# Performance work log

Hardware: AMD Instinct MI355X
Metric: run time of the kernel (lower is better)

## Reference

```python
import jax, jax.numpy as jnp
import numpy as np
import math

EPS = 1e-5
L2_EPS = 1e-12  # torch F.normalize default eps


def _bitlinear(x, W):
    """BitNet b1.58-style BitLinear: ternary weights (per-tensor mean-abs scale)
    and per-token int8 absmax activation quantization. No bias.
    x: [..., in], W: [out, in] -> [..., out]
    """
    w_scale = jnp.clip(jnp.mean(jnp.abs(W)), EPS, None)
    W_q = jnp.clip(jnp.round(W / w_scale), -1.0, 1.0) * w_scale
    x_scale = 127.0 / jnp.clip(jnp.max(jnp.abs(x), axis=-1, keepdims=True), EPS, None)
    x_q = jnp.clip(jnp.round(x * x_scale), -128.0, 127.0) / x_scale
    return jnp.einsum('bsi,oi->bso', x_q, W_q)


def setup_inputs() -> dict:
    key = jax.random.key(0)
    k1, k2, k3 = jax.random.split(key, 3)
    B, S, D_in, P, D_out = 4, 4096, 2048, 16, 2048
    x = jax.random.normal(k1, (B, S, D_in), dtype=jnp.float32)
    # xavier_normal_: std = sqrt(2 / (fan_in + fan_out))
    Wk = jax.random.normal(k2, (P, D_in), dtype=jnp.float32) * math.sqrt(2.0 / (D_in + P))
    Wv = jax.random.normal(k3, (D_out, P), dtype=jnp.float32) * math.sqrt(2.0 / (P + D_out))
    return {"x": x, "Wk": Wk, "Wv": Wv}


def reference(x, Wk, Wv):
    # key projection -> [B, S, P]
    attn = _bitlinear(x, Wk)
    # gelu (exact erf form, torch default) + L2-normalize * sqrt(P)
    attn = jax.nn.gelu(attn, approximate=False)
    norm = jnp.clip(jnp.linalg.norm(attn, axis=-1, keepdims=True), L2_EPS, None)
    attn = attn / norm * jnp.sqrt(jnp.float32(attn.shape[-1]))
    # value projection -> [B, S, D_out]
    return _bitlinear(attn, Wv)
```

## Files before the change

kernel.cpp:

```cpp
#include <hip/hip_runtime.h>

#define DIN   2048
#define DOUT  2048
#define NP    16
#define TPW   8
#define WPB   2

#define HDR_OFF   0
#define WK4_OFF   256
#define WV4_OFF   (WK4_OFF + 32768)

static __device__ __forceinline__ int dot4(unsigned a, unsigned b, int c) {
#if defined(__has_builtin) && __has_builtin(__builtin_amdgcn_sdot4)
  return __builtin_amdgcn_sdot4((int)a, (int)b, c, false);
#else
  c += (int)(signed char)(a & 0xffu)        * (int)(signed char)(b & 0xffu);
  c += (int)(signed char)((a >> 8) & 0xffu) * (int)(signed char)((b >> 8) & 0xffu);
  c += (int)(signed char)((a >> 16) & 0xffu)* (int)(signed char)((b >> 16) & 0xffu);
  c += (int)(signed char)(a >> 24)          * (int)(signed char)(b >> 24);
  return c;
#endif
}

static __device__ __forceinline__ unsigned qmagic(float f, float xs) {
  return __float_as_uint(fmaf(f, xs, 12582912.0f)) & 0xffu;
}

static __device__ __forceinline__ unsigned q8(float f, float xs) {
  float t = f * xs;
  float r = rintf(t);
  r = fmaxf(-128.0f, fminf(127.0f, r));
  return ((unsigned)(int)r) & 0xffu;
}

__global__ __launch_bounds__(256) void k_prep(
    const float* __restrict__ Wk, const float* __restrict__ Wv,
    float* __restrict__ hdr, unsigned* __restrict__ wk4, unsigned* __restrict__ wv4)
{
  __shared__ float red[8][256];
  const int tid = threadIdx.x, b = blockIdx.x;
  const int isV = (b >= 32);
  const float4* W = (const float4*)(isV ? Wv : Wk);

  float4 own = make_float4(0.f, 0.f, 0.f, 0.f);
#pragma unroll
  for (int lb = 0; lb < 8; ++lb) {
    float s = 0.f;
#pragma unroll
    for (int i = 0; i < 4; ++i) {
      float4 v = W[lb * 1024 + i * 256 + tid];
      if (!isV && (lb * 4 + i) == b) own = v;
      s += fabsf(v.x) + fabsf(v.y) + fabsf(v.z) + fabsf(v.w);
    }
    red[lb][tid] = s;
  }
  __syncthreads();
#pragma unroll 1
  for (int o = 128; o > 0; o >>= 1) {
    if (tid < o) {
#pragma unroll
      for (int lb = 0; lb < 8; ++lb) red[lb][tid] += red[lb][tid + o];
    }
    __syncthreads();
  }
  float sum = 0.f;
#pragma unroll
  for (int lb = 0; lb < 8; ++lb) sum += red[lb][0];
  const float sc = fmaxf(sum * (1.0f / 32768.0f), 1e-5f);
  if (tid == 0 && (b == 0 || b == 32)) hdr[isV] = sc;

  if (!isV) {
    const int c = b * 256 + tid;
    unsigned pk = 0; const float* wp = &own.x;
#pragma unroll
    for (int j = 0; j < 4; ++j) {
      float r = rintf(wp[j] / sc);
      r = fmaxf(-1.0f, fminf(1.0f, r));
      pk |= (((unsigned)(int)r) & 0xffu) << (8 * j);
    }
    wk4[c] = pk;
  } else {
    const int o = (b - 32) * 256 + tid;
    unsigned u[4];
#pragma unroll
    for (int cc = 0; cc < 4; ++cc) {
      float4 w = ((const float4*)Wv)[o * 4 + cc];
      const float* wp = &w.x;
      unsigned pk = 0;
#pragma unroll
      for (int r = 0; r < 4; ++r) {
        float q = rintf(wp[r] / sc);
        q = fmaxf(-1.0f, fminf(1.0f, q));
        pk |= (((unsigned)(int)q) & 0xffu) << (8 * r);
      }
      u[cc] = pk;
    }
    ((uint4*)wv4)[o] = make_uint4(u[0], u[1], u[2], u[3]);
  }
}

__global__ __launch_bounds__(128, 2) void k_main(
    const float* __restrict__ x, const float* __restrict__ hdr,
    const unsigned* __restrict__ wk4, const unsigned* __restrict__ wv4,
    float* __restrict__ out)
{
  const int l  = threadIdx.x & 63;
  const int ws = threadIdx.x >> 6;
  const long t0 = ((long)blockIdx.x * WPB + ws) * TPW;

  __shared__ uint4 qls[WPB][TPW];
  __shared__ float sls[WPB][TPW];

  const float w1 = hdr[0], w2 = hdr[1];
  const float4* xf = (const float4*)x;

  unsigned tab[128];
#pragma unroll
  for (int p = 0; p < 16; ++p)
#pragma unroll
    for (int c = 0; c < 8; ++c) tab[p * 8 + c] = wk4[p * 512 + c * 64 + l];

  float4 a[2][8];
#pragma unroll
  for (int c = 0; c < 8; ++c) a[0][c] = xf[t0 * 512 + c * 64 + l];

#pragma unroll 1
  for (int g = 0; g < TPW / 4; ++g) {
    int   sv[4];
    float s1[4];
#pragma unroll
    for (int ii = 0; ii < 4; ++ii) {
      const long tok = t0 + g * 4 + ii;

      float mx = 0.0f;
#pragma unroll
      for (int c = 0; c < 8; ++c) {
        float4 v = a[ii & 1][c];
        mx = fmaxf(mx, fabsf(v.x)); mx = fmaxf(mx, fabsf(v.y));
        mx = fmaxf(mx, fabsf(v.z)); mx = fmaxf(mx, fabsf(v.w));
      }
#pragma unroll
      for (int d = 1; d < 64; d <<= 1) mx = fmaxf(mx, __shfl_xor(mx, d, 64));
      const float mcl = fmaxf(mx, 1e-5f);
      const float xs  = 127.0f / mcl;
      s1[ii] = w1 / xs;

      unsigned qp[8];
#pragma unroll
      for (int c = 0; c < 8; ++c) {
        float4 v = a[ii & 1][c];
        qp[c] = qmagic(v.x, xs) | (qmagic(v.y, xs) << 8)
              | (qmagic(v.z, xs) << 16) | (qmagic(v.w, xs) << 24);
      }

      if (g * 4 + ii < TPW - 1) {
#pragma unroll
        for (int c = 0; c < 8; ++c)
          a[(ii + 1) & 1][c] = xf[(tok + 1) * 512 + c * 64 + l];
      }

      int acc[16];
#pragma unroll
      for (int p = 0; p < 16; ++p) {
        int d = 0;
#pragma unroll
        for (int c = 0; c < 8; ++c) d = dot4(qp[c], tab[p * 8 + c], d);
        acc[p] = d;
      }

#pragma unroll
      for (int b = 0; b < 4; ++b) {
        const int lb = (l >> b) & 1;
#pragma unroll
        for (int j = 0; j < 8; ++j) {
          if (j < (8 >> b)) {
            int keep = lb ? acc[2 * j + 1] : acc[2 * j];
            int send = lb ? acc[2 * j]     : acc[2 * j + 1];
            acc[j] = keep + __shfl_xor(send, 1 << b, 64);
          }
        }
      }
      sv[ii] = acc[0];
    }

    const int lb4 = (l >> 4) & 1, lb5 = (l >> 5) & 1;
    int r0 = (lb4 ? sv[1] : sv[0]) + __shfl_xor(lb4 ? sv[0] : sv[1], 16, 64);
    int r1 = (lb4 ? sv[3] : sv[2]) + __shfl_xor(lb4 ? sv[2] : sv[3], 16, 64);
    int rr = (lb5 ? r1 : r0) + __shfl_xor(lb5 ? r0 : r1, 32, 64);
    float s1a = lb4 ? s1[1] : s1[0];
    float s1b = lb4 ? s1[3] : s1[2];
    const float s1sel = lb5 ? s1b : s1a;

    const float fa = (float)rr * s1sel;
    const float gv = 0.5f * fa * (1.0f + erff(fa * 0.70710678118654752f));
    float ss = gv * gv;
    ss += __shfl_xor(ss, 1, 64); ss += __shfl_xor(ss, 2, 64);
    ss += __shfl_xor(ss, 4, 64); ss += __shfl_xor(ss, 8, 64);
    const float rn = fmaxf(sqrtf(ss), 1e-12f);
    const float gn = gv * (4.0f / rn);
    float am = fabsf(gn);
    {
      float o;
      o = __shfl_xor(am, 1, 64); am = fmaxf(am, o);
      o = __shfl_xor(am, 2, 64); am = fmaxf(am, o);
      o = __shfl_xor(am, 4, 64); am = fmaxf(am, o);
      o = __shfl_xor(am, 8, 64); am = fmaxf(am, o);
    }
    const float mc2 = fmaxf(am, 1e-5f);
    const float xs2 = 127.0f / mc2;
    const float s2  = w2 / xs2;

    unsigned sh = q8(gn, xs2) << ((l & 3) * 8);
    sh |= (unsigned)__shfl_xor((int)sh, 1, 64);
    sh |= (unsigned)__shfl_xor((int)sh, 2, 64);
    const unsigned wa = (unsigned)__shfl_xor((int)sh, 4, 64);
    const unsigned wb = (unsigned)__shfl_xor((int)sh, 8, 64);
    const unsigned wc = (unsigned)__shfl_xor((int)sh, 12, 64);
    if ((l & 15) == 0) {
      qls[ws][g * 4 + (l >> 4)] = make_uint4(sh, wa, wb, wc);
      sls[ws][g * 4 + (l >> 4)] = s2;
    }
  }

#pragma unroll
  for (int m = 0; m < 8; ++m)
#pragma unroll
    for (int j = 0; j < 4; ++j) {
      uint4 t = ((const uint4*)wv4)[m * 256 + l * 4 + j];
      tab[(m * 4 + j) * 4 + 0] = t.x; tab[(m * 4 + j) * 4 + 1] = t.y;
      tab[(m * 4 + j) * 4 + 2] = t.z; tab[(m * 4 + j) * 4 + 3] = t.w;
    }

  __syncthreads();

  for (int i = 0; i < TPW; ++i) {
    const long tok = t0 + i;
    const uint4 q  = qls[ws][i];
    const float s2 = sls[ws][i];
#pragma unroll
    for (int m = 0; m < 8; ++m) {
      float h[4];
#pragma unroll
      for (int j = 0; j < 4; ++j) {
        int d = dot4(q.x, tab[(m * 4 + j) * 4 + 0], 0);
        d = dot4(q.y, tab[(m * 4 + j) * 4 + 1], d);
        d = dot4(q.z, tab[(m * 4 + j) * 4 + 2], d);
        d = dot4(q.w, tab[(m * 4 + j) * 4 + 3], d);
        h[j] = (float)d * s2;
      }
      *(float4*)(out + (size_t)tok * 2048 + m * 256 + l * 4) =
          make_float4(h[0], h[1], h[2], h[3]);
    }
  }
}

extern "C" void kernel_launch(void* const* d_in, const int* in_sizes, int n_in,
                              void* d_out, int out_size, void* d_ws, size_t ws_size,
                              hipStream_t stream) {
  const float* x  = (const float*)d_in[0];
  const float* Wk = (const float*)d_in[1];
  const float* Wv = (const float*)d_in[2];

  const int tokens = in_sizes[0] / DIN;

  char* ws = (char*)d_ws;
  float*    hdr = (float*)(ws + HDR_OFF);
  unsigned* wk4 = (unsigned*)(ws + WK4_OFF);
  unsigned* wv4 = (unsigned*)(ws + WV4_OFF);

  k_prep<<<40, 256, 0, stream>>>(Wk, Wv, hdr, wk4, wv4);
  k_main<<<tokens / (TPW * WPB), 128, 0, stream>>>(x, hdr, wk4, wv4, (float*)d_out);
}
```

Measured before the change: 248.9 us.

## Stage ternary weight tables in LDS instead of per-thread registers

Moves the packed Wk and Wv ternary tables out of a 128-entry per-thread register array into shared memory, loaded cooperatively once per 256-thread block (4 waves), and reorders the value projection to loop over weights outside tokens. This frees a large register footprint to raise occupancy and lets each LDS weight load be reused across 8 tokens. In exchange it adds 64KB of LDS per block, which limits blocks per CU, and puts LDS reads in the inner dot loops.

```diff
diff --git a/kernel.cpp b/kernel.cpp
--- a/kernel.cpp
+++ b/kernel.cpp
@@ -4,7 +4,7 @@
 #define DOUT  2048
 #define NP    16
 #define TPW   8
-#define WPB   2
+#define WPB   4
 
 #define HDR_OFF   0
 #define WK4_OFF   256
@@ -99,30 +99,46 @@
   }
 }
 
-__global__ __launch_bounds__(128, 2) void k_main(
+__global__ __launch_bounds__(256) void k_main(
     const float* __restrict__ x, const float* __restrict__ hdr,
     const unsigned* __restrict__ wk4, const unsigned* __restrict__ wv4,
     float* __restrict__ out)
 {
-  const int l  = threadIdx.x & 63;
-  const int ws = threadIdx.x >> 6;
+  const int tid = threadIdx.x;
+  const int l   = tid & 63;
+  const int ws  = tid >> 6;
   const long t0 = ((long)blockIdx.x * WPB + ws) * TPW;
 
+  __shared__ uint4 wkL[2048];
+  __shared__ uint4 wvL[2048];
   __shared__ uint4 qls[WPB][TPW];
   __shared__ float sls[WPB][TPW];
 
   const float w1 = hdr[0], w2 = hdr[1];
   const float4* xf = (const float4*)x;
 
-  unsigned tab[128];
-#pragma unroll
-  for (int p = 0; p < 16; ++p)
-#pragma unroll
-    for (int c = 0; c < 8; ++c) tab[p * 8 + c] = wk4[p * 512 + c * 64 + l];
-
   float4 a[2][8];
 #pragma unroll
   for (int c = 0; c < 8; ++c) a[0][c] = xf[t0 * 512 + c * 64 + l];
+
+  {
+    unsigned* wkW = (unsigned*)wkL;
+#pragma unroll
+    for (int i = 0; i < 32; ++i) {
+      const int g = i * 256 + tid;
+      const unsigned v = wk4[g];
+      const int p = g >> 9, rem = g & 511, c = rem >> 6, lg = rem & 63;
+      wkW[p * 512 + (c >> 2) * 256 + lg * 4 + (c & 3)] = v;
+    }
+#pragma unroll
+    for (int i = 0; i < 8; ++i) {
+      const int o = i * 256 + tid;
+      const uint4 v = ((const uint4*)wv4)[o];
+      const int m = o >> 8, r = o & 255, lr = r >> 2, j = r & 3;
+      wvL[(m * 4 + j) * 64 + lr] = v;
+    }
+  }
+  __syncthreads();
 
 #pragma unroll 1
   for (int g = 0; g < TPW / 4; ++g) {
@@ -162,9 +178,13 @@
       int acc[16];
 #pragma unroll
       for (int p = 0; p < 16; ++p) {
+        const uint4 w0 = wkL[p * 128 + l];
+        const uint4 w4 = wkL[p * 128 + 64 + l];
         int d = 0;
-#pragma unroll
-        for (int c = 0; c < 8; ++c) d = dot4(qp[c], tab[p * 8 + c], d);
+        d = dot4(qp[0], w0.x, d); d = dot4(qp[1], w0.y, d);
+        d = dot4(qp[2], w0.z, d); d = dot4(qp[3], w0.w, d);
+        d = dot4(qp[4], w4.x, d); d = dot4(qp[5], w4.y, d);
+        d = dot4(qp[6], w4.z, d); d = dot4(qp[7], w4.w, d);
         acc[p] = d;
       }
 
@@ -222,34 +242,29 @@
     }
   }
 
-#pragma unroll
-  for (int m = 0; m < 8; ++m)
+  uint4 q[TPW]; float s2v[TPW];
+#pragma unroll
+  for (int i = 0; i < TPW; ++i) { q[i] = qls[ws][i]; s2v[i] = sls[ws][i]; }
+
+#pragma unroll
+  for (int m = 0; m < 8; ++m) {
+    float h[TPW][4];
 #pragma unroll
     for (int j = 0; j < 4; ++j) {
-      uint4 t = ((const uint4*)wv4)[m * 256 + l * 4 + j];
-      tab[(m * 4 + j) * 4 + 0] = t.x; tab[(m * 4 + j) * 4 + 1] = t.y;
-      tab[(m * 4 + j) * 4 + 2] = t.z; tab[(m * 4 + j) * 4 + 3] = t.w;
-    }
-
-  __syncthreads();
-
-  for (int i = 0; i < TPW; ++i) {
-    const long tok = t0 + i;
-    const uint4 q  = qls[ws][i];
-    const float s2 = sls[ws][i];
-#pragma unroll
-    for (int m = 0; m < 8; ++m) {
-      float h[4];
-#pragma unroll
-      for (int j = 0; j < 4; ++j) {
-        int d = dot4(q.x, tab[(m * 4 + j) * 4 + 0], 0);
-        d = dot4(q.y, tab[(m * 4 + j) * 4 + 1], d);
-        d = dot4(q.z, tab[(m * 4 + j) * 4 + 2], d);
-        d = dot4(q.w, tab[(m * 4 + j) * 4 + 3], d);
-        h[j] = (float)d * s2;
-      }
-      *(float4*)(out + (size_t)tok * 2048 + m * 256 + l * 4) =
-          make_float4(h[0], h[1], h[2], h[3]);
+      const uint4 w = wvL[(m * 4 + j) * 64 + l];
+#pragma unroll
+      for (int t = 0; t < TPW; ++t) {
+        int d = dot4(q[t].x, w.x, 0);
+        d = dot4(q[t].y, w.y, d);
+        d = dot4(q[t].z, w.z, d);
+        d = dot4(q[t].w, w.w, d);
+        h[t][j] = (float)d * s2v[t];
+      }
+    }
+#pragma unroll
+    for (int t = 0; t < TPW; ++t) {
+      *(float4*)(out + (size_t)(t0 + t) * 2048 + m * 256 + l * 4) =
+          make_float4(h[t][0], h[t][1], h[t][2], h[t][3]);
     }
   }
 }
@@ -269,5 +284,5 @@
   unsigned* wv4 = (unsigned*)(ws + WV4_OFF);
 
   k_prep<<<40, 256, 0, stream>>>(Wk, Wv, hdr, wk4, wv4);
-  k_main<<<tokens / (TPW * WPB), 128, 0, stream>>>(x, hdr, wk4, wv4, (float*)d_out);
-}
+  k_main<<<tokens / (TPW * WPB), 256, 0, stream>>>(x, hdr, wk4, wv4, (float*)d_out);
+}
```

New measurement: 249.4 us. About the same (+0.2%).
